# Kernel tuning notes

Hardware: AMD Instinct MI355X
Metric: run time of the kernel (lower is better)

## Reference

```python
import jax, jax.numpy as jnp
import numpy as np

B, S, D, H = 4, 2048, 1024, 16
HD = D // H


def setup_inputs() -> dict:
    key = jax.random.key(0)
    ks = jax.random.split(key, 12)
    sc = 0.02
    inp = {
        "q": jax.random.normal(ks[0], (B, S, D), jnp.float32),
        "k": jax.random.normal(ks[1], (B, S, D), jnp.float32),
        "v": jax.random.normal(ks[2], (B, S, D), jnp.float32),
        "mask": jnp.tril(jnp.ones((S, S), jnp.int32))[None, None],  # causal [1,1,S,S]
        "Wq": jax.random.normal(ks[3], (D, D), jnp.float32) * sc,
        "bq": jnp.zeros((D,), jnp.float32),
        "Wk": jax.random.normal(ks[4], (D, D), jnp.float32) * sc,
        "bk": jnp.zeros((D,), jnp.float32),
        "Wv": jax.random.normal(ks[5], (D, D), jnp.float32) * sc,
        "bv": jnp.zeros((D,), jnp.float32),
        "Wo": jax.random.normal(ks[6], (D, D), jnp.float32) * sc,
        "bo": jnp.zeros((D,), jnp.float32),
    }
    return inp


def reference(q, k, v, mask, Wq, bq, Wk, bk, Wv, bv, Wo, bo):
    # Linear projections (torch Linear: x @ W.T + b)
    qh = (q @ Wq.T + bq).reshape(B, S, H, HD).transpose(0, 2, 1, 3)  # [B,H,S,hd]
    kh = (k @ Wk.T + bk).reshape(B, S, H, HD).transpose(0, 2, 1, 3)
    vh = (v @ Wv.T + bv).reshape(B, S, H, HD).transpose(0, 2, 1, 3)
    score = jnp.einsum("bhqd,bhkd->bhqk", qh, kh) / jnp.sqrt(jnp.float32(HD))
    score = jnp.where(mask == 0, jnp.float32(-10000.0), score)
    attn = jax.nn.softmax(score, axis=-1)
    out = jnp.einsum("bhqk,bhkd->bhqd", attn, vh)  # [B,H,S,hd]
    out = out.transpose(0, 2, 1, 3).reshape(B, S, D)
    return out @ Wo.T + bo
```

## Files before the change

### kernel.cpp

```cpp
#include <hip/hip_runtime.h>

#define S_LEN 2048
#define D_DIM 1024
#define NB    4
#define NH    16
#define HDIM  64
#define QSCL  0.18033688011112042f

typedef float  f32x4  __attribute__((ext_vector_type(4)));
typedef __bf16 bf16x4 __attribute__((ext_vector_type(4)));
typedef __bf16 bf16x8 __attribute__((ext_vector_type(8)));

static __device__ __forceinline__ f32x4 mfma16(bf16x8 a, bf16x8 b, f32x4 c) {
  return __builtin_amdgcn_mfma_f32_16x16x32_bf16(a, b, c, 0, 0, 0);
}
static __device__ __forceinline__ bf16x4 cvt4(f32x4 v) {
  return __builtin_convertvector(v, bf16x4);
}
static __device__ __forceinline__ bf16x8 cvt8(f32x4 lo, f32x4 hi) {
  bf16x4 a = cvt4(lo), b = cvt4(hi);
  bf16x8 r;
  r[0] = a[0]; r[1] = a[1]; r[2] = a[2]; r[3] = a[3];
  r[4] = b[0]; r[5] = b[1]; r[6] = b[2]; r[7] = b[3];
  return r;
}
static __device__ __forceinline__ void cp16(const void* g, void* l) {
  __builtin_amdgcn_global_load_lds(
      (const __attribute__((address_space(1))) unsigned int*)g,
      (__attribute__((address_space(3))) unsigned int*)l, 16, 0, 0);
}

__global__ __launch_bounds__(256) void conv_w(
    const float* __restrict__ Wq, const float* __restrict__ Wk,
    const float* __restrict__ Wv, const float* __restrict__ Wo,
    __bf16* __restrict__ out)
{
  const float* src;
  if (blockIdx.y == 0) src = Wq;
  else if (blockIdx.y == 1) src = Wk;
  else if (blockIdx.y == 2) src = Wv;
  else src = Wo;
  size_t i = ((size_t)blockIdx.x * 256 + threadIdx.x) * 4;
  f32x4 v = *(const f32x4*)(src + i);
  *(bf16x4*)(out + (size_t)blockIdx.y * (D_DIM * D_DIM) + i) = cvt4(v);
}

static __device__ __forceinline__ void proj_epilogue(
    f32x4 (&acc)[4][4], int z, int mbase, int nbase, int wm, int wn,
    int l15, int quad, const float* bias,
    __bf16* qh, __bf16* kh, __bf16* vt)
{
  const float scl = (z == 0) ? QSCL : 1.0f;
#pragma unroll
  for (int mt = 0; mt < 4; ++mt)
#pragma unroll
    for (int nt = 0; nt < 4; ++nt) {
      int n = nbase + wn + nt * 16 + l15;
      int h = n >> 6, hd = n & 63;
      float bb = bias[n];
      f32x4 vv = acc[mt][nt];
#pragma unroll
      for (int r = 0; r < 4; ++r) vv[r] = (vv[r] + bb) * scl;
      bf16x4 pv = cvt4(vv);
      int m0 = mbase + wm + mt * 16 + quad * 4;
      int b = m0 >> 11, s0 = m0 & 2047;
      if (z == 2) {
        *(bf16x4*)(vt + ((size_t)((b * NH + h) * HDIM + hd)) * S_LEN + s0) = pv;
      } else {
        __bf16* out = (z == 0) ? qh : kh;
#pragma unroll
        for (int r = 0; r < 4; ++r)
          out[((size_t)(b * NH + h) * S_LEN + s0 + r) * HDIM + hd] = pv[r];
      }
    }
}

__global__ __launch_bounds__(256, 4) void proj_fused(
    const float* __restrict__ qin, const float* __restrict__ kin,
    const float* __restrict__ vin, const __bf16* __restrict__ Wbf,
    const float* __restrict__ bq, const float* __restrict__ bk, const float* __restrict__ bv,
    __bf16* __restrict__ qh, __bf16* __restrict__ kh, __bf16* __restrict__ vt)
{
  const float* A; const float* bias;
  if (blockIdx.z == 0)      { A = qin; bias = bq; }
  else if (blockIdx.z == 1) { A = kin; bias = bk; }
  else                      { A = vin; bias = bv; }
  const __bf16* W = Wbf + (size_t)blockIdx.z * (D_DIM * D_DIM);

  __shared__ __bf16 As[128 * 64];
  __shared__ __bf16 Bs[128 * 64];

  const int tid  = threadIdx.x;
  const int wave = tid >> 6;
  const int lane = tid & 63;
  const int l15  = lane & 15;
  const int quad = lane >> 4;
  const int mbase = blockIdx.x * 128;
  const int nbase = blockIdx.y * 128;
  const int wm = (wave & 1) * 64;
  const int wn = (wave >> 1) * 64;
  const int brow = lane >> 3;
  const int scol = ((lane & 7) ^ (brow & 7)) * 8;
  const int swz  = l15 & 7;

  f32x4 acc[4][4] = {};

  for (int kt = 0; kt < D_DIM; kt += 64) {
#pragma unroll
    for (int c = 0; c < 4; ++c) {
      int r = wave * 32 + c * 8 + brow;
      cp16(W + (size_t)(nbase + r) * D_DIM + kt + scol, Bs + r * 64);
    }
    {
      f32x4 a0[4], a1[4];
#pragma unroll
      for (int c = 0; c < 4; ++c) {
        const float* src = A + (size_t)(mbase + wave * 32 + c * 8 + brow) * D_DIM
                           + kt + scol;
        a0[c] = *(const f32x4*)(src);
        a1[c] = *(const f32x4*)(src + 4);
      }
#pragma unroll
      for (int c = 0; c < 4; ++c) {
        int r = wave * 32 + c * 8 + brow;
        *(bf16x8*)(As + r * 64 + (lane & 7) * 8) = cvt8(a0[c], a1[c]);
      }
    }
    __syncthreads();

#pragma unroll
    for (int k0 = 0; k0 < 2; ++k0) {
      bf16x8 af[4], bfr[4];
#pragma unroll
      for (int i = 0; i < 4; ++i) {
        int off = ((k0 * 4 + quad) ^ swz) * 8;
        af[i]  = *(const bf16x8*)(As + (wm + i * 16 + l15) * 64 + off);
        bfr[i] = *(const bf16x8*)(Bs + (wn + i * 16 + l15) * 64 + off);
      }
#pragma unroll
      for (int mt = 0; mt < 4; ++mt)
#pragma unroll
        for (int nt = 0; nt < 4; ++nt)
          acc[mt][nt] = mfma16(af[mt], bfr[nt], acc[mt][nt]);
    }
    __syncthreads();
  }

  proj_epilogue(acc, blockIdx.z, mbase, nbase, wm, wn, l15, quad, bias, qh, kh, vt);
}

__global__ __launch_bounds__(256, 4) void attn_kernel(
    const __bf16* __restrict__ qh, const __bf16* __restrict__ kh,
    const __bf16* __restrict__ vt, __bf16* __restrict__ ao)
{
  __shared__ __bf16 Kb[2][64 * 64];
  __shared__ __bf16 Vb[2][64 * 64];

  const int lin = blockIdx.x + (blockIdx.y << 4);
  const int xcd = lin & 7;
  const int idx = lin >> 3;
  const int u   = idx & 15;
  const int x   = (u & 1) ? (15 - (u >> 1)) : (u >> 1);
  const int bh  = xcd * 8 + (idx >> 4);

  const int qc0 = x, qc1 = 31 - x;
  const int last = qc1;

  const __bf16* qp = qh + (size_t)bh * S_LEN * HDIM;
  const __bf16* kp = kh + (size_t)bh * S_LEN * HDIM;
  const __bf16* vp = vt + (size_t)bh * HDIM * S_LEN;

  const int tid  = threadIdx.x;
  const int wave = tid >> 6;
  const int lane = tid & 63;
  const int l15  = lane & 15;
  const int quad = lane >> 4;
  const int w16  = wave * 16;
  const int srow = lane >> 3;
  const int swz  = l15 & 7;
  const int vswz = ((l15 >> 3) << 2) | (l15 & 3);
  const int kr0  = ((l15 >> 2) << 3) | (l15 & 3);
  const int b = bh >> 4, h = bh & 15;

  bf16x8 fq[2][2];
#pragma unroll
  for (int j = 0; j < 2; ++j) {
    const int qb = (j ? qc1 : qc0) * 64;
    const __bf16* qrow = qp + (size_t)(qb + w16 + l15) * HDIM;
    fq[j][0] = *(const bf16x8*)(qrow + quad * 8);
    fq[j][1] = *(const bf16x8*)(qrow + 32 + quad * 8);
  }

  f32x4 accO[2][4] = {};
  float lp[2] = {0.f, 0.f};

#pragma unroll
  for (int c = 0; c < 2; ++c) {
    int rb = w16 + c * 8;
    int sc2 = (((lane & 7) ^ (((c & 1) << 2) | (srow & 3)))) * 8;
    cp16(kp + (size_t)(rb + srow) * HDIM + sc2, &Kb[0][rb * 64]);
    cp16(vp + (size_t)(rb + srow) * S_LEN + sc2, &Vb[0][rb * 64]);
  }

  int cur = 0;
  for (int kt = 0; kt <= last; ++kt) {
    __syncthreads();

    if (kt < last) {
#pragma unroll
      for (int c = 0; c < 2; ++c) {
        int rb = w16 + c * 8;
        int sc2 = (((lane & 7) ^ (((c & 1) << 2) | (srow & 3)))) * 8;
        cp16(kp + (size_t)((kt + 1) * 64 + rb + srow) * HDIM + sc2,
             &Kb[cur ^ 1][rb * 64]);
        cp16(vp + (size_t)(rb + srow) * S_LEN + (kt + 1) * 64 + sc2,
             &Vb[cur ^ 1][rb * 64]);
      }
    }

    const __bf16* Kc = &Kb[cur][0];
    const __bf16* Vc = &Vb[cur][0];
    const bool act0 = (kt <= qc0);

    f32x4 sc[2][4] = {};
    __builtin_amdgcn_s_setprio(1);
#pragma unroll
    for (int k0 = 0; k0 < 2; ++k0)
#pragma unroll
      for (int nt = 0; nt < 4; ++nt) {
        const int krow = kr0 + ((nt & 1) << 2) + ((nt >> 1) << 5);
        bf16x8 bk = *(const bf16x8*)(Kc + krow * 64 +
                                     (((k0 * 4 + quad) ^ swz) * 8));
        if (act0) sc[0][nt] = mfma16(bk, fq[0][k0], sc[0][nt]);
        sc[1][nt] = mfma16(bk, fq[1][k0], sc[1][nt]);
      }
    __builtin_amdgcn_s_setprio(0);

    bf16x8 pa[2][2];
#pragma unroll
    for (int j = 0; j < 2; ++j) {
      if (j == 0 && !act0) continue;
      const int qcj = j ? qc1 : qc0;
      f32x4 pf[4];
#pragma unroll
      for (int nt = 0; nt < 4; ++nt) {
#pragma unroll
        for (int r = 0; r < 4; ++r) pf[nt][r] = __builtin_amdgcn_exp2f(sc[j][nt][r]);
        if (kt == qcj) {
#pragma unroll
          for (int r = 0; r < 4; ++r) {
            int key = ((nt >> 1) << 5) + (quad << 3) + ((nt & 1) << 2) + r;
            if (key > w16 + l15) pf[nt][r] = 0.f;
          }
        }
      }
      f32x4 lv = (pf[0] + pf[1]) + (pf[2] + pf[3]);
      lp[j] += (lv[0] + lv[1]) + (lv[2] + lv[3]);
      pa[j][0] = cvt8(pf[0], pf[1]);
      pa[j][1] = cvt8(pf[2], pf[3]);
    }

    __builtin_amdgcn_s_setprio(1);
#pragma unroll
    for (int k0 = 0; k0 < 2; ++k0)
#pragma unroll
      for (int nt = 0; nt < 4; ++nt) {
        bf16x8 bv = *(const bf16x8*)(Vc + (nt * 16 + l15) * 64 +
                                     (((k0 * 4 + quad) ^ vswz) * 8));
        if (act0) accO[0][nt] = mfma16(pa[0][k0], bv, accO[0][nt]);
        accO[1][nt] = mfma16(pa[1][k0], bv, accO[1][nt]);
      }
    __builtin_amdgcn_s_setprio(0);

    cur ^= 1;
  }

#pragma unroll
  for (int j = 0; j < 2; ++j) {
    float lf = lp[j];
    lf += __shfl_xor(lf, 16);
    lf += __shfl_xor(lf, 32);
    const int qb = (j ? qc1 : qc0) * 64;
#pragma unroll
    for (int r = 0; r < 4; ++r) {
      float inv = 1.0f / __shfl(lf, quad * 4 + r);
#pragma unroll
      for (int nt = 0; nt < 4; ++nt) accO[j][nt][r] *= inv;
    }
#pragma unroll
    for (int nt = 0; nt < 4; ++nt) {
      bf16x4 ob = cvt4(accO[j][nt]);
#pragma unroll
      for (int r = 0; r < 4; ++r) {
        int sr = qb + w16 + quad * 4 + r;
        ao[((size_t)b * S_LEN + sr) * D_DIM + h * HDIM + nt * 16 + l15] = ob[r];
      }
    }
  }
}

__global__ __launch_bounds__(256, 4) void out_gemm(
    const __bf16* __restrict__ Ain, const __bf16* __restrict__ Wbf,
    const float* __restrict__ bo, float* __restrict__ Cout)
{
  __shared__ __bf16 As[128 * 64];
  __shared__ __bf16 Bs[128 * 64];

  const int tid  = threadIdx.x;
  const int wave = tid >> 6;
  const int lane = tid & 63;
  const int l15  = lane & 15;
  const int quad = lane >> 4;
  const int mbase = blockIdx.x * 128;
  const int nbase = blockIdx.y * 128;
  const int wm = (wave & 1) * 64;
  const int wn = (wave >> 1) * 64;
  const int brow = lane >> 3;
  const int scol = ((lane & 7) ^ (brow & 7)) * 8;
  const int swz  = l15 & 7;

  f32x4 acc[4][4] = {};

  for (int kt = 0; kt < D_DIM; kt += 64) {
#pragma unroll
    for (int c = 0; c < 4; ++c) {
      int r = wave * 32 + c * 8 + brow;
      cp16(Ain + (size_t)(mbase + r) * D_DIM + kt + scol, As + r * 64);
      cp16(Wbf + (size_t)(nbase + r) * D_DIM + kt + scol, Bs + r * 64);
    }
    __syncthreads();

#pragma unroll
    for (int k0 = 0; k0 < 2; ++k0) {
      bf16x8 af[4], bfr[4];
#pragma unroll
      for (int i = 0; i < 4; ++i) {
        int off = ((k0 * 4 + quad) ^ swz) * 8;
        af[i]  = *(const bf16x8*)(As + (wm + i * 16 + l15) * 64 + off);
        bfr[i] = *(const bf16x8*)(Bs + (wn + i * 16 + l15) * 64 + off);
      }
#pragma unroll
      for (int mt = 0; mt < 4; ++mt)
#pragma unroll
        for (int nt = 0; nt < 4; ++nt)
          acc[mt][nt] = mfma16(af[mt], bfr[nt], acc[mt][nt]);
    }
    __syncthreads();
  }

#pragma unroll
  for (int mt = 0; mt < 4; ++mt)
#pragma unroll
    for (int nt = 0; nt < 4; ++nt) {
      int n = nbase + wn + nt * 16 + l15;
      float bb = bo[n];
      int m0 = mbase + wm + mt * 16 + quad * 4;
#pragma unroll
      for (int r = 0; r < 4; ++r)
        Cout[(size_t)(m0 + r) * D_DIM + n] = acc[mt][nt][r] + bb;
    }
}

extern "C" void kernel_launch(void* const* d_in, const int* in_sizes, int n_in,
                              void* d_out, int out_size, void* d_ws, size_t ws_size,
                              hipStream_t stream) {
  const float* q  = (const float*)d_in[0];
  const float* k  = (const float*)d_in[1];
  const float* v  = (const float*)d_in[2];
  const float* Wq = (const float*)d_in[4];
  const float* bq = (const float*)d_in[5];
  const float* Wk = (const float*)d_in[6];
  const float* bk = (const float*)d_in[7];
  const float* Wv = (const float*)d_in[8];
  const float* bv = (const float*)d_in[9];
  const float* Wo = (const float*)d_in[10];
  const float* bo = (const float*)d_in[11];

  __bf16* ws = (__bf16*)d_ws;
  const size_t WSZ = (size_t)D_DIM * D_DIM;
  const size_t NE  = (size_t)NB * S_LEN * D_DIM;
  __bf16* wbf = ws;
  __bf16* qh  = ws + 4 * WSZ;
  __bf16* kh  = qh + NE;
  __bf16* vt  = kh + NE;
  __bf16* ao  = vt + NE;

  conv_w<<<dim3(1024, 4), 256, 0, stream>>>(Wq, Wk, Wv, Wo, wbf);
  proj_fused<<<dim3(64, 8, 3), 256, 0, stream>>>(q, k, v, wbf, bq, bk, bv, qh, kh, vt);
  attn_kernel<<<dim3(16, 64), 256, 0, stream>>>(qh, kh, vt, ao);
  out_gemm<<<dim3(64, 8), 256, 0, stream>>>(ao, wbf + 3 * WSZ, bo, (float*)d_out);
}
```

Measured before the change: 317.3 us.

## Pre-convert activations to bf16 and use async LDS loads in projection GEMM

Adds a conversion pass that writes bf16 copies of q, k and v alongside the weight conversion. The projection GEMM can then stream its A tiles through global_load_lds, just as it already does for the weights, instead of doing fp32 register loads and in-kernel conversion. Block indices in the projection and output GEMMs are remapped so neighbouring tiles land on the same XCD for better L2 reuse. The cost is an extra full read of the fp32 activations plus a bf16 write. The bf16 activation buffer starts at the attention-output workspace slot and spans three activation-sized regions, so it relies on the workspace being large enough and on the buffer being dead once projection finishes.

```diff
diff --git a/kernel.cpp b/kernel.cpp
--- a/kernel.cpp
+++ b/kernel.cpp
@@ -17,32 +17,33 @@
 static __device__ __forceinline__ bf16x4 cvt4(f32x4 v) {
   return __builtin_convertvector(v, bf16x4);
 }
-static __device__ __forceinline__ bf16x8 cvt8(f32x4 lo, f32x4 hi) {
-  bf16x4 a = cvt4(lo), b = cvt4(hi);
-  bf16x8 r;
-  r[0] = a[0]; r[1] = a[1]; r[2] = a[2]; r[3] = a[3];
-  r[4] = b[0]; r[5] = b[1]; r[6] = b[2]; r[7] = b[3];
-  return r;
-}
 static __device__ __forceinline__ void cp16(const void* g, void* l) {
   __builtin_amdgcn_global_load_lds(
       (const __attribute__((address_space(1))) unsigned int*)g,
       (__attribute__((address_space(3))) unsigned int*)l, 16, 0, 0);
 }
 
-__global__ __launch_bounds__(256) void conv_w(
+__global__ __launch_bounds__(256) void conv_all(
+    const float* __restrict__ q, const float* __restrict__ k,
+    const float* __restrict__ v,
     const float* __restrict__ Wq, const float* __restrict__ Wk,
     const float* __restrict__ Wv, const float* __restrict__ Wo,
-    __bf16* __restrict__ out)
-{
-  const float* src;
-  if (blockIdx.y == 0) src = Wq;
-  else if (blockIdx.y == 1) src = Wk;
-  else if (blockIdx.y == 2) src = Wv;
-  else src = Wo;
-  size_t i = ((size_t)blockIdx.x * 256 + threadIdx.x) * 4;
-  f32x4 v = *(const f32x4*)(src + i);
-  *(bf16x4*)(out + (size_t)blockIdx.y * (D_DIM * D_DIM) + i) = cvt4(v);
+    __bf16* __restrict__ abf, __bf16* __restrict__ wbf)
+{
+  const int y = blockIdx.y;
+  if (y < 3) {
+    const float* src = (y == 0) ? q : (y == 1) ? k : v;
+    size_t i = ((size_t)blockIdx.x * 256 + threadIdx.x) * 4;
+    f32x4 x = *(const f32x4*)(src + i);
+    *(bf16x4*)(abf + (size_t)y * ((size_t)NB * S_LEN * D_DIM) + i) = cvt4(x);
+  } else {
+    if (blockIdx.x >= 4096) return;
+    const int w = blockIdx.x >> 10;
+    const float* src = (w == 0) ? Wq : (w == 1) ? Wk : (w == 2) ? Wv : Wo;
+    size_t i = ((size_t)(blockIdx.x & 1023) * 256 + threadIdx.x) * 4;
+    f32x4 x = *(const f32x4*)(src + i);
+    *(bf16x4*)(wbf + (size_t)w * (D_DIM * D_DIM) + i) = cvt4(x);
+  }
 }
 
 static __device__ __forceinline__ void proj_epilogue(
@@ -75,17 +76,21 @@
     }
 }
 
-__global__ __launch_bounds__(256, 4) void proj_fused(
-    const float* __restrict__ qin, const float* __restrict__ kin,
-    const float* __restrict__ vin, const __bf16* __restrict__ Wbf,
+__global__ __launch_bounds__(256, 4) void proj_bf16(
+    const __bf16* __restrict__ abf, const __bf16* __restrict__ Wbf,
     const float* __restrict__ bq, const float* __restrict__ bk, const float* __restrict__ bv,
     __bf16* __restrict__ qh, __bf16* __restrict__ kh, __bf16* __restrict__ vt)
 {
-  const float* A; const float* bias;
-  if (blockIdx.z == 0)      { A = qin; bias = bq; }
-  else if (blockIdx.z == 1) { A = kin; bias = bk; }
-  else                      { A = vin; bias = bv; }
-  const __bf16* W = Wbf + (size_t)blockIdx.z * (D_DIM * D_DIM);
+  const int lin = blockIdx.x + (blockIdx.y << 6) + (blockIdx.z << 9);
+  const int wg  = (lin & 7) * 192 + (lin >> 3);
+  const int z   = wg >> 9;
+  const int rem = wg & 511;
+  const int xg  = rem >> 3;
+  const int yg  = rem & 7;
+
+  const __bf16* A = abf + (size_t)z * ((size_t)NB * S_LEN * D_DIM);
+  const __bf16* W = Wbf + (size_t)z * (D_DIM * D_DIM);
+  const float* bias = (z == 0) ? bq : (z == 1) ? bk : bv;
 
   __shared__ __bf16 As[128 * 64];
   __shared__ __bf16 Bs[128 * 64];
@@ -95,8 +100,8 @@
   const int lane = tid & 63;
   const int l15  = lane & 15;
   const int quad = lane >> 4;
-  const int mbase = blockIdx.x * 128;
-  const int nbase = blockIdx.y * 128;
+  const int mbase = xg * 128;
+  const int nbase = yg * 128;
   const int wm = (wave & 1) * 64;
   const int wn = (wave >> 1) * 64;
   const int brow = lane >> 3;
@@ -109,22 +114,8 @@
 #pragma unroll
     for (int c = 0; c < 4; ++c) {
       int r = wave * 32 + c * 8 + brow;
+      cp16(A + (size_t)(mbase + r) * D_DIM + kt + scol, As + r * 64);
       cp16(W + (size_t)(nbase + r) * D_DIM + kt + scol, Bs + r * 64);
-    }
-    {
-      f32x4 a0[4], a1[4];
-#pragma unroll
-      for (int c = 0; c < 4; ++c) {
-        const float* src = A + (size_t)(mbase + wave * 32 + c * 8 + brow) * D_DIM
-                           + kt + scol;
-        a0[c] = *(const f32x4*)(src);
-        a1[c] = *(const f32x4*)(src + 4);
-      }
-#pragma unroll
-      for (int c = 0; c < 4; ++c) {
-        int r = wave * 32 + c * 8 + brow;
-        *(bf16x8*)(As + r * 64 + (lane & 7) * 8) = cvt8(a0[c], a1[c]);
-      }
     }
     __syncthreads();
 
@@ -146,7 +137,7 @@
     __syncthreads();
   }
 
-  proj_epilogue(acc, blockIdx.z, mbase, nbase, wm, wn, l15, quad, bias, qh, kh, vt);
+  proj_epilogue(acc, z, mbase, nbase, wm, wn, l15, quad, bias, qh, kh, vt);
 }
 
 __global__ __launch_bounds__(256, 4) void attn_kernel(
@@ -256,8 +247,14 @@
       }
       f32x4 lv = (pf[0] + pf[1]) + (pf[2] + pf[3]);
       lp[j] += (lv[0] + lv[1]) + (lv[2] + lv[3]);
-      pa[j][0] = cvt8(pf[0], pf[1]);
-      pa[j][1] = cvt8(pf[2], pf[3]);
+      bf16x4 c0 = cvt4(pf[0]), c1 = cvt4(pf[1]), c2 = cvt4(pf[2]), c3 = cvt4(pf[3]);
+      bf16x8 p0, p1;
+      p0[0]=c0[0]; p0[1]=c0[1]; p0[2]=c0[2]; p0[3]=c0[3];
+      p0[4]=c1[0]; p0[5]=c1[1]; p0[6]=c1[2]; p0[7]=c1[3];
+      p1[0]=c2[0]; p1[1]=c2[1]; p1[2]=c2[2]; p1[3]=c2[3];
+      p1[4]=c3[0]; p1[5]=c3[1]; p1[6]=c3[2]; p1[7]=c3[3];
+      pa[j][0] = p0;
+      pa[j][1] = p1;
     }
 
     __builtin_amdgcn_s_setprio(1);
@@ -303,6 +300,11 @@
     const __bf16* __restrict__ Ain, const __bf16* __restrict__ Wbf,
     const float* __restrict__ bo, float* __restrict__ Cout)
 {
+  const int lin = blockIdx.x + (blockIdx.y << 6);
+  const int wg  = (lin & 7) * 64 + (lin >> 3);
+  const int xg  = wg >> 3;
+  const int yg  = wg & 7;
+
   __shared__ __bf16 As[128 * 64];
   __shared__ __bf16 Bs[128 * 64];
 
@@ -311,8 +313,8 @@
   const int lane = tid & 63;
   const int l15  = lane & 15;
   const int quad = lane >> 4;
-  const int mbase = blockIdx.x * 128;
-  const int nbase = blockIdx.y * 128;
+  const int mbase = xg * 128;
+  const int nbase = yg * 128;
   const int wm = (wave & 1) * 64;
   const int wn = (wave >> 1) * 64;
   const int brow = lane >> 3;
@@ -384,9 +386,10 @@
   __bf16* kh  = qh + NE;
   __bf16* vt  = kh + NE;
   __bf16* ao  = vt + NE;
-
-  conv_w<<<dim3(1024, 4), 256, 0, stream>>>(Wq, Wk, Wv, Wo, wbf);
-  proj_fused<<<dim3(64, 8, 3), 256, 0, stream>>>(q, k, v, wbf, bq, bk, bv, qh, kh, vt);
+  __bf16* abf = vt + NE;
+
+  conv_all<<<dim3(8192, 4), 256, 0, stream>>>(q, k, v, Wq, Wk, Wv, Wo, abf, wbf);
+  proj_bf16<<<dim3(64, 8, 3), 256, 0, stream>>>(abf, wbf, bq, bk, bv, qh, kh, vt);
   attn_kernel<<<dim3(16, 64), 256, 0, stream>>>(qh, kh, vt, ao);
   out_gemm<<<dim3(64, 8), 256, 0, stream>>>(ao, wbf + 3 * WSZ, bo, (float*)d_out);
 }
```

Result: faster. 300.4 us (median of 2 runs) (-5.3%).
